# Kernel tuning notes

Hardware: AMD Instinct MI355X
Metric: run time of the kernel (lower is better)

The kernel has to match this reference:

```python
import jax, jax.numpy as jnp
import numpy as np

NBINS = 256


def _getmask(mi):
    # mi: [h, w] image already scaled to [0, 255]
    # torch.histc(mi, bins=256, min=0, max=255): values outside [0,255] ignored
    hist = jax.lax.stop_gradient(
        jnp.histogram(mi, bins=NBINS, range=(0.0, 255.0))[0].astype(jnp.float32)
    )
    # mask_output[i] = sum_j |j - i| * hist[j]  -> small 256x256 matvec
    j = jnp.arange(NBINS, dtype=jnp.float32)
    dist = jnp.abs(j[:, None] - j[None, :])  # [256, 256]
    mask_output = dist @ hist                 # [256]
    # mask[image==i] = mask_output[i]; only exact-integer pixels in [0,255] match
    r = jnp.round(mi)
    valid = (mi == r) & (r >= 0.0) & (r <= 255.0)
    idx = jnp.clip(r, 0.0, 255.0).astype(jnp.int32)
    mask = jnp.where(valid, mask_output[idx], 0.0)
    # if mask.max()==0: return zeros; else return the (scaled) image itself
    return jnp.where(mask.max() == 0.0, jnp.zeros_like(mi), mi)


def _forward(image_irr, image_vis):
    irr = image_irr * 255.0
    _vis = image_vis * 255.0  # computed but unused in the original forward
    mi = irr[:, 0, :, :]                       # [b, h, w]
    masked = jax.vmap(_getmask)(mi) / 255.0    # [b, h, w]
    msk_ir = masked[:, None, :, :]             # [b, 1, h, w]
    msk = jnp.stack([msk_ir, 1.0 - msk_ir], axis=0)  # [2, b, 1, h, w]
    msks = jax.nn.softmax(msk, axis=0)
    return msks[0], msks[1]


def setup_inputs() -> dict:
    key = jax.random.key(0)
    k1, k2 = jax.random.split(key)
    shape = (16, 1, 1024, 1024)
    # quantized pixels so that image*255 is (mostly) exactly integer,
    # matching the module's implicit assumption (histc + equality tests)
    image_irr = jax.random.randint(k1, shape, 0, 256).astype(jnp.float32) / 255.0
    image_vis = jax.random.randint(k2, shape, 0, 256).astype(jnp.float32) / 255.0
    return {"image_irr": image_irr, "image_vis": image_vis}


def reference(image_irr, image_vis):
    return _forward(image_irr, image_vis)
```

## Files before the change

### kernel.cpp

```cpp
#include <hip/hip_runtime.h>
#include <stdint.h>

#define NBINS 256
#define BATCH 16
#define HW (1024*1024)
#define NPIX (BATCH * HW)

__global__ __launch_bounds__(256) void hist_kernel(const float* __restrict__ in,
                                                   unsigned* __restrict__ ghist,
                                                   unsigned* __restrict__ gvhist) {
    __shared__ unsigned sh[NBINS];
    const int tid = threadIdx.x;
    const int batch = blockIdx.y;
    for (int i = tid; i < NBINS; i += 256) sh[i] = 0;
    __syncthreads();

    const float4* src = (const float4*)(in + (size_t)batch * HW) + (size_t)blockIdx.x * 4096;
    for (int i = tid; i < 4096; i += 256) {
        float4 x = src[i];
        float v[4] = {x.x, x.y, x.z, x.w};
#pragma unroll
        for (int k = 0; k < 4; ++k) {
            float mi = v[k] * 255.0f;
            if (mi >= 0.0f && mi <= 255.0f) {
                int b = (int)(mi * (256.0f / 255.0f));
                if (b > 255) b = 255;
                float r = rintf(mi);
                unsigned add = (mi == r) ? 0x10001u : 1u;
                atomicAdd(&sh[b], add);
            }
        }
    }
    __syncthreads();
    for (int i = tid; i < NBINS; i += 256) {
        unsigned p = sh[i];
        if (p) {
            atomicAdd(&ghist[batch * NBINS + i], p & 0xFFFFu);
            atomicAdd(&gvhist[batch * NBINS + i], p >> 16);
        }
    }
}

__global__ __launch_bounds__(256) void flag_kernel(const unsigned* __restrict__ ghist,
                                                   const unsigned* __restrict__ gvhist,
                                                   unsigned* __restrict__ flags) {
    __shared__ unsigned stot[NBINS];
    __shared__ int any;
    const int b = blockIdx.x;
    const int j = threadIdx.x;
    unsigned h = ghist[b * NBINS + j];
    unsigned v = gvhist[b * NBINS + j];
    if (j == 0) any = 0;
    stot[j] = h;
    __syncthreads();
    for (int s = 128; s > 0; s >>= 1) {
        if (j < s) stot[j] += stot[j + s];
        __syncthreads();
    }
    unsigned total = stot[0];
    if (v > 0 && total > h) any = 1;
    __syncthreads();
    if (j == 0) flags[b] = (unsigned)any;
}

__device__ __forceinline__ void softmax2(float x, unsigned flag, float& o0, float& o1) {
    float mi = x * 255.0f;
    float m = flag ? (mi / 255.0f) : 0.0f;
    float a = m;
    float b = 1.0f - m;
    float M = fmaxf(a, b);
    float e0 = expf(a - M);
    float e1 = expf(b - M);
    float s = e0 + e1;
    o0 = e0 / s;
    o1 = e1 / s;
}

__global__ __launch_bounds__(256) void out_kernel(const float* __restrict__ in,
                                                  const unsigned* __restrict__ flags,
                                                  float* __restrict__ out) {
    const size_t i4 = (size_t)blockIdx.x * 256 + threadIdx.x;
    const int batch = (int)(i4 >> 18);
    const unsigned f = flags[batch];
    float4 x = ((const float4*)in)[i4];
    float4 o0, o1;
    softmax2(x.x, f, o0.x, o1.x);
    softmax2(x.y, f, o0.y, o1.y);
    softmax2(x.z, f, o0.z, o1.z);
    softmax2(x.w, f, o0.w, o1.w);
    ((float4*)out)[i4] = o0;
    ((float4*)(out + (size_t)NPIX))[i4] = o1;
}

extern "C" void kernel_launch(void* const* d_in, const int* in_sizes, int n_in,
                              void* d_out, int out_size, void* d_ws, size_t ws_size,
                              hipStream_t stream) {
    const float* irr = (const float*)d_in[0];
    float* out = (float*)d_out;

    unsigned* ghist  = (unsigned*)d_ws;
    unsigned* gvhist = ghist + BATCH * NBINS;
    unsigned* flags  = gvhist + BATCH * NBINS;

    hipMemsetAsync(d_ws, 0, (size_t)(2 * BATCH * NBINS + BATCH) * sizeof(unsigned), stream);

    hist_kernel<<<dim3(64, BATCH), 256, 0, stream>>>(irr, ghist, gvhist);
    flag_kernel<<<BATCH, 256, 0, stream>>>(ghist, gvhist, flags);
    out_kernel<<<NPIX / 4 / 256, 256, 0, stream>>>(irr, flags, out);
}
```

Before: 231.3 us.

## Replace histogram with min/max bin and validity reduction for mask flag

The shared-memory atomic histogram becomes a per-block min/max bin index plus a validity OR, reduced with a tree in shared memory and then wave shuffles in the flag kernel. The mask is nonzero when some valid integer pixel exists and the histogram is not concentrated in a single bin, which is the same as requiring more than one occupied bin. Removing the atomics eliminates contention on hot bins, and the workspace memset goes away because every partial is written directly. It depends on that equivalence holding, including how invalid pixels are counted.

```diff
diff --git a/kernel.cpp b/kernel.cpp
--- a/kernel.cpp
+++ b/kernel.cpp
@@ -5,15 +5,17 @@
 #define BATCH 16
 #define HW (1024*1024)
 #define NPIX (BATCH * HW)
+#define SCAN_BLOCKS 64
 
-__global__ __launch_bounds__(256) void hist_kernel(const float* __restrict__ in,
-                                                   unsigned* __restrict__ ghist,
-                                                   unsigned* __restrict__ gvhist) {
-    __shared__ unsigned sh[NBINS];
+__global__ __launch_bounds__(256) void scan_kernel(const float* __restrict__ in,
+                                                   uint2* __restrict__ partials) {
+    __shared__ int smin[256], smax[256];
+    __shared__ unsigned sval[256];
     const int tid = threadIdx.x;
     const int batch = blockIdx.y;
-    for (int i = tid; i < NBINS; i += 256) sh[i] = 0;
-    __syncthreads();
+
+    int minb = 0x7FFF, maxb = -1;
+    unsigned valid = 0;
 
     const float4* src = (const float4*)(in + (size_t)batch * HW) + (size_t)blockIdx.x * 4096;
     for (int i = tid; i < 4096; i += 256) {
@@ -25,42 +27,45 @@
             if (mi >= 0.0f && mi <= 255.0f) {
                 int b = (int)(mi * (256.0f / 255.0f));
                 if (b > 255) b = 255;
-                float r = rintf(mi);
-                unsigned add = (mi == r) ? 0x10001u : 1u;
-                atomicAdd(&sh[b], add);
+                minb = min(minb, b);
+                maxb = max(maxb, b);
+                valid |= (mi == rintf(mi)) ? 1u : 0u;
             }
         }
     }
+    smin[tid] = minb; smax[tid] = maxb; sval[tid] = valid;
     __syncthreads();
-    for (int i = tid; i < NBINS; i += 256) {
-        unsigned p = sh[i];
-        if (p) {
-            atomicAdd(&ghist[batch * NBINS + i], p & 0xFFFFu);
-            atomicAdd(&gvhist[batch * NBINS + i], p >> 16);
+    for (int s = 128; s > 0; s >>= 1) {
+        if (tid < s) {
+            smin[tid] = min(smin[tid], smin[tid + s]);
+            smax[tid] = max(smax[tid], smax[tid + s]);
+            sval[tid] |= sval[tid + s];
         }
+        __syncthreads();
+    }
+    if (tid == 0) {
+        uint2 p;
+        p.x = ((unsigned)(smin[0] & 0xFFFF) << 16) | (unsigned)(smax[0] & 0xFFFF);
+        p.y = sval[0];
+        partials[batch * SCAN_BLOCKS + blockIdx.x] = p;
     }
 }
 
-__global__ __launch_bounds__(256) void flag_kernel(const unsigned* __restrict__ ghist,
-                                                   const unsigned* __restrict__ gvhist,
-                                                   unsigned* __restrict__ flags) {
-    __shared__ unsigned stot[NBINS];
-    __shared__ int any;
+__global__ __launch_bounds__(64) void flag_kernel(const uint2* __restrict__ partials,
+                                                  unsigned* __restrict__ flags) {
     const int b = blockIdx.x;
-    const int j = threadIdx.x;
-    unsigned h = ghist[b * NBINS + j];
-    unsigned v = gvhist[b * NBINS + j];
-    if (j == 0) any = 0;
-    stot[j] = h;
-    __syncthreads();
-    for (int s = 128; s > 0; s >>= 1) {
-        if (j < s) stot[j] += stot[j + s];
-        __syncthreads();
+    const int t = threadIdx.x;
+    uint2 p = partials[b * SCAN_BLOCKS + t];
+    int minb = (int)(short)(p.x >> 16);
+    int maxb = (int)(short)(p.x & 0xFFFF);
+    unsigned valid = p.y;
+#pragma unroll
+    for (int off = 32; off > 0; off >>= 1) {
+        minb = min(minb, __shfl_xor(minb, off));
+        maxb = max(maxb, __shfl_xor(maxb, off));
+        valid |= (unsigned)__shfl_xor((int)valid, off);
     }
-    unsigned total = stot[0];
-    if (v > 0 && total > h) any = 1;
-    __syncthreads();
-    if (j == 0) flags[b] = (unsigned)any;
+    if (t == 0) flags[b] = (valid && (minb != maxb)) ? 1u : 0u;
 }
 
 __device__ __forceinline__ void softmax2(float x, unsigned flag, float& o0, float& o1) {
@@ -98,13 +103,10 @@
     const float* irr = (const float*)d_in[0];
     float* out = (float*)d_out;
 
-    unsigned* ghist  = (unsigned*)d_ws;
-    unsigned* gvhist = ghist + BATCH * NBINS;
-    unsigned* flags  = gvhist + BATCH * NBINS;
+    uint2* partials = (uint2*)d_ws;
+    unsigned* flags = (unsigned*)(partials + BATCH * SCAN_BLOCKS);
 
-    hipMemsetAsync(d_ws, 0, (size_t)(2 * BATCH * NBINS + BATCH) * sizeof(unsigned), stream);
-
-    hist_kernel<<<dim3(64, BATCH), 256, 0, stream>>>(irr, ghist, gvhist);
-    flag_kernel<<<BATCH, 256, 0, stream>>>(ghist, gvhist, flags);
+    scan_kernel<<<dim3(SCAN_BLOCKS, BATCH), 256, 0, stream>>>(irr, partials);
+    flag_kernel<<<BATCH, 64, 0, stream>>>(partials, flags);
     out_kernel<<<NPIX / 4 / 256, 256, 0, stream>>>(irr, flags, out);
 }
```

Result: no change. 230.5 us (-0.3%).
